# Performance work log

Hardware: AMD Instinct MI355X
Metric: run time of the kernel (lower is better)

The kernel has to match this reference:

```python
import jax, jax.numpy as jnp
import numpy as np

P = 2          # patch size
DEPTH = 3
NHEAD = 8
DROP_RATIO = 0.15
LN_EPS = 1e-5


def _ln(x, g, b):
    m = jnp.mean(x, axis=-1, keepdims=True)
    v = jnp.mean((x - m) ** 2, axis=-1, keepdims=True)
    return (x - m) * jax.lax.rsqrt(v + LN_EPS) * g + b


def setup_inputs() -> dict:
    key = jax.random.key(0)
    ks = jax.random.split(key, 16)
    B, C, HW, D, L = 4, 3, 96, 256, DEPTH
    N = (HW // P) ** 2
    s = 0.02
    return {
        "x": jax.random.normal(ks[0], (B, C, HW, HW), jnp.float32),
        "patch_w": jax.random.normal(ks[1], (D, C, P, P), jnp.float32) * s,
        "patch_b": jnp.zeros((D,), jnp.float32),
        "pos": jax.random.normal(ks[2], (1, N, D), jnp.float32) * s,
        "imp_w1": jax.random.normal(ks[3], (D, 256), jnp.float32) * s,
        "imp_b1": jnp.zeros((256,), jnp.float32),
        "imp_w2": jax.random.normal(ks[4], (256, 1), jnp.float32) * s,
        "imp_b2": jnp.zeros((1,), jnp.float32),
        "ln1_g": jnp.ones((L, D), jnp.float32),
        "ln1_b": jnp.zeros((L, D), jnp.float32),
        "qkv_w": jax.random.normal(ks[5], (L, D, 3 * D), jnp.float32) * s,
        "qkv_b": jnp.zeros((L, 3 * D), jnp.float32),
        "proj_w": jax.random.normal(ks[6], (L, D, D), jnp.float32) * s,
        "proj_b": jnp.zeros((L, D), jnp.float32),
        "ln2_g": jnp.ones((L, D), jnp.float32),
        "ln2_b": jnp.zeros((L, D), jnp.float32),
        "mlp_w1": jax.random.normal(ks[7], (L, D, 4 * D), jnp.float32) * s,
        "mlp_b1": jnp.zeros((L, 4 * D), jnp.float32),
        "mlp_w2": jax.random.normal(ks[8], (L, 4 * D, D), jnp.float32) * s,
        "mlp_b2": jnp.zeros((L, D), jnp.float32),
        "out_g": jnp.ones((D,), jnp.float32),
        "out_b": jnp.zeros((D,), jnp.float32),
    }


def reference(x, patch_w, patch_b, pos, imp_w1, imp_b1, imp_w2, imp_b2,
              ln1_g, ln1_b, qkv_w, qkv_b, proj_w, proj_b,
              ln2_g, ln2_b, mlp_w1, mlp_b1, mlp_w2, mlp_b2, out_g, out_b):
    B, C, H, W = x.shape
    D = patch_w.shape[0]
    Hc, Wc = H // P, W // P
    # Patch embed: conv(k=stride=P) == blocked einsum  -> (B, N, D)
    xr = x.reshape(B, C, Hc, P, Wc, P)
    tokens = jnp.einsum('bchpwq,dcpq->bhwd', xr, patch_w).reshape(B, Hc * Wc, D) + patch_b
    tokens = tokens + pos
    B, N, _ = tokens.shape

    # Importance scores -> bottom-k keys masked (Eq.8-10)
    h = jax.nn.relu(tokens @ imp_w1 + imp_b1)
    scores = jax.nn.sigmoid((h @ imp_w2 + imp_b2)[..., 0])  # (B, N)
    k = int(DROP_RATIO * N)
    _, idx = jax.lax.top_k(-scores, k)                      # k smallest scores
    md = jnp.zeros((B, N), bool).at[jnp.arange(B)[:, None], idx].set(True)

    dk = D // NHEAD
    scale = 1.0 / np.sqrt(dk)
    for l in range(DEPTH):
        hln = _ln(tokens, ln1_g[l], ln1_b[l])
        qkv = hln @ qkv_w[l] + qkv_b[l]
        q, kk, v = jnp.split(qkv, 3, axis=-1)
        q = q.reshape(B, N, NHEAD, dk).transpose(0, 2, 1, 3)
        kk = kk.reshape(B, N, NHEAD, dk).transpose(0, 2, 1, 3)
        v = v.reshape(B, N, NHEAD, dk).transpose(0, 2, 1, 3)
        logits = jnp.einsum('bhnd,bhmd->bhnm', q, kk) * scale
        logits = jnp.where(md[:, None, None, :], -jnp.inf, logits)
        attn = jax.nn.softmax(logits, axis=-1)
        out = jnp.einsum('bhnm,bhmd->bhnd', attn, v)
        out = out.transpose(0, 2, 1, 3).reshape(B, N, D)
        tokens = tokens + (out @ proj_w[l] + proj_b[l])
        h2 = _ln(tokens, ln2_g[l], ln2_b[l])
        tokens = tokens + (jax.nn.gelu(h2 @ mlp_w1[l] + mlp_b1[l], approximate=False) @ mlp_w2[l] + mlp_b2[l])

    tokens = _ln(tokens, out_g, out_b)
    return tokens.mean(axis=1)  # (B, D)
```

## Files before the change

### kernel.cpp

```cpp
#include <hip/hip_runtime.h>
#include <hip/hip_bf16.h>
#include <math.h>

#define BATCH 4
#define NTOK  2304
#define DIM   256
#define NHEADS 8
#define HCDIM 48
#define KSEL  345
#define NKEEP 1959
#define NKC   1984
#define KT    31
#define KREM  39
#define LN_EPS 1e-5f

typedef unsigned short u16;
typedef __attribute__((ext_vector_type(8))) short bf16x8;
typedef __attribute__((ext_vector_type(4))) float f32x4;

__device__ __forceinline__ u16 f2bf(float x) {
  union { float f; unsigned u; } v; v.f = x;
  return (u16)((v.u + 0x7FFFu + ((v.u >> 16) & 1u)) >> 16);
}

__device__ __forceinline__ void gload_lds16(const u16* g, u16* l) {
  __builtin_amdgcn_global_load_lds((const __attribute__((address_space(1))) void*)g,
                                   (__attribute__((address_space(3))) void*)l, 16, 0, 0);
}

__global__ __launch_bounds__(256) void k_patch_embed(
    const float* __restrict__ x, const float* __restrict__ pw,
    const float* __restrict__ pb, const float* __restrict__ pos,
    float* __restrict__ tokens) {
  int blk = blockIdx.x;
  int b = blk / NTOK, n = blk % NTOK;
  int hc = n / HCDIM, wc = n % HCDIM;
  __shared__ float xs[12];
  int t = threadIdx.x;
  if (t < 12) {
    int c = t >> 2, p = (t >> 1) & 1, q = t & 1;
    xs[t] = x[((b * 3 + c) * 96 + (hc * 2 + p)) * 96 + (wc * 2 + q)];
  }
  __syncthreads();
  float acc = pb[t];
#pragma unroll
  for (int i = 0; i < 12; ++i) acc += xs[i] * pw[t * 12 + i];
  tokens[(size_t)(b * NTOK + n) * DIM + t] = acc + pos[n * DIM + t];
}

__global__ __launch_bounds__(256) void k_importance(
    const float* __restrict__ tokens, const float* __restrict__ w1,
    const float* __restrict__ b1, const float* __restrict__ w2,
    const float* __restrict__ b2, float* __restrict__ scores) {
  __shared__ float ts[16 * 256];
  __shared__ float hw[16 * 256];
  int base = blockIdx.x * 16;
  int t = threadIdx.x;
  for (int i = t; i < 16 * 256; i += 256) ts[i] = tokens[(size_t)base * 256 + i];
  __syncthreads();
  float acc[16];
#pragma unroll
  for (int r = 0; r < 16; ++r) acc[r] = b1[t];
  for (int i = 0; i < 256; ++i) {
    float w = w1[i * 256 + t];
#pragma unroll
    for (int r = 0; r < 16; ++r) acc[r] += ts[r * 256 + i] * w;
  }
  float w2v = w2[t];
#pragma unroll
  for (int r = 0; r < 16; ++r) hw[r * 256 + t] = fmaxf(acc[r], 0.f) * w2v;
  __syncthreads();
  if (t < 16) {
    float s = b2[0];
    for (int i = 0; i < 256; ++i) s += hw[t * 256 + i];
    scores[base + t] = 1.f / (1.f + expf(-s));
  }
}

__global__ __launch_bounds__(256) void k_select(const float* __restrict__ scores,
                                                int* __restrict__ cmap,
                                                u16* __restrict__ kvc) {
  int b = blockIdx.x, t = threadIdx.x;
  __shared__ unsigned sb[NTOK];
  __shared__ int cnt;
  __shared__ int pfl[256], pfe[256];
  __shared__ int remS;
  for (int i = t; i < NTOK; i += 256) sb[i] = __float_as_uint(scores[b * NTOK + i]);
  __syncthreads();
  unsigned prefix = 0;
  int r = KSEL;
  for (int bit = 31; bit >= 0; --bit) {
    if (t == 0) cnt = 0;
    __syncthreads();
    unsigned bmask = 1u << bit;
    unsigned hmask = (bit == 31) ? 0u : ~((bmask << 1) - 1u);
    int local = 0;
    for (int i = t; i < NTOK; i += 256)
      if ((sb[i] & hmask) == prefix && !(sb[i] & bmask)) local++;
    if (local) atomicAdd(&cnt, local);
    __syncthreads();
    int c0 = cnt;
    if (r > c0) { r -= c0; prefix |= bmask; }
    __syncthreads();
  }
  unsigned v = prefix;
  int cl = 0, ce = 0;
  int j0 = t * 9;
  for (int j = j0; j < j0 + 9; ++j) { cl += (sb[j] < v); ce += (sb[j] == v); }
  pfl[t] = cl; pfe[t] = ce;
  __syncthreads();
  if (t == 0) {
    int pl = 0, pe = 0;
    for (int i = 0; i < 256; ++i) {
      int a = pfl[i], e = pfe[i];
      pfl[i] = pl; pfe[i] = pe;
      pl += a; pe += e;
    }
    remS = KSEL - pl;
  }
  __syncthreads();
  int pl = pfl[t], pe = pfe[t], rem = remS;
  for (int j = j0; j < j0 + 9; ++j) {
    bool less = sb[j] < v, eq = sb[j] == v;
    bool drop = less || (eq && pe < rem);
    int dropped_before = pl + (pe < rem ? pe : rem);
    cmap[b * NTOK + j] = drop ? -1 : (j - dropped_before);
    pl += less; pe += eq;
  }
  for (int i = t; i < (NKC - NKEEP) * 512; i += 256)
    kvc[((size_t)b * NKC + NKEEP) * 512 + i] = 0;
}

__global__ __launch_bounds__(256) void k_ln4bf(
    const float* __restrict__ in, u16* __restrict__ out,
    const float* __restrict__ g, const float* __restrict__ bta) {
  int w = threadIdx.x >> 6, l = threadIdx.x & 63;
  size_t row = (size_t)blockIdx.x * 4 + w;
  float4 v = *(const float4*)(in + row * DIM + l * 4);
  float s = v.x + v.y + v.z + v.w;
  float ss = v.x * v.x + v.y * v.y + v.z * v.z + v.w * v.w;
#pragma unroll
  for (int o = 1; o < 64; o <<= 1) { s += __shfl_xor(s, o); ss += __shfl_xor(ss, o); }
  float m = s * (1.f / DIM);
  float inv = rsqrtf(ss * (1.f / DIM) - m * m + LN_EPS);
  float4 gv = *(const float4*)(g + l * 4);
  float4 bv = *(const float4*)(bta + l * 4);
  union { ushort4 u4; __hip_bfloat162 h2[2]; } o4;
  o4.h2[0] = __float22bfloat162_rn(make_float2((v.x - m) * inv * gv.x + bv.x,
                                               (v.y - m) * inv * gv.y + bv.y));
  o4.h2[1] = __float22bfloat162_rn(make_float2((v.z - m) * inv * gv.z + bv.z,
                                               (v.w - m) * inv * gv.w + bv.w));
  *(ushort4*)(out + row * DIM + l * 4) = o4.u4;
}

__global__ __launch_bounds__(256) void k_lnmean(
    const float* __restrict__ in, const float* __restrict__ g,
    const float* __restrict__ bta, float* __restrict__ part) {
  int chunk = blockIdx.x, b = blockIdx.y;
  int w = threadIdx.x >> 6, l = threadIdx.x & 63;
  float4 gv = *(const float4*)(g + l * 4);
  float4 bv = *(const float4*)(bta + l * 4);
  float4 acc = make_float4(0.f, 0.f, 0.f, 0.f);
  for (int i = 0; i < 16; ++i) {
    size_t row = (size_t)b * NTOK + chunk * 64 + w * 16 + i;
    float4 v = *(const float4*)(in + row * DIM + l * 4);
    float s = v.x + v.y + v.z + v.w;
    float ss = v.x * v.x + v.y * v.y + v.z * v.z + v.w * v.w;
#pragma unroll
    for (int o = 1; o < 64; o <<= 1) { s += __shfl_xor(s, o); ss += __shfl_xor(ss, o); }
    float m = s * (1.f / DIM);
    float inv = rsqrtf(ss * (1.f / DIM) - m * m + LN_EPS);
    acc.x += (v.x - m) * inv * gv.x + bv.x;
    acc.y += (v.y - m) * inv * gv.y + bv.y;
    acc.z += (v.z - m) * inv * gv.z + bv.z;
    acc.w += (v.w - m) * inv * gv.w + bv.w;
  }
  __shared__ float4 red[4][64];
  red[w][l] = acc;
  __syncthreads();
  if (w == 0) {
    float4 a0 = red[0][l], a1 = red[1][l], a2 = red[2][l], a3 = red[3][l];
    float4 tot = make_float4(a0.x + a1.x + a2.x + a3.x, a0.y + a1.y + a2.y + a3.y,
                             a0.z + a1.z + a2.z + a3.z, a0.w + a1.w + a2.w + a3.w);
    *(float4*)(part + ((size_t)b * 36 + chunk) * DIM + l * 4) = tot;
  }
}

__global__ __launch_bounds__(256) void k_mean_final(const float* __restrict__ part,
                                                    float* __restrict__ out) {
  int b = blockIdx.x, d = threadIdx.x;
  float s = 0.f;
  for (int c = 0; c < 36; ++c) s += part[(size_t)(b * 36 + c) * DIM + d];
  out[b * DIM + d] = s * (1.0f / NTOK);
}

__global__ __launch_bounds__(256) void k_wtrans_all(
    const float* __restrict__ qkv_w, const float* __restrict__ proj_w,
    const float* __restrict__ mlp_w1, const float* __restrict__ mlp_w2,
    u16* __restrict__ wq, u16* __restrict__ wp,
    u16* __restrict__ w1, u16* __restrict__ w2) {
  int id = blockIdx.x;
  const float* W; u16* WT; int K, N, m;
  if (id < 576)       { m = id;        K = 256;  N = 768;  W = qkv_w;  WT = wq; }
  else if (id < 768)  { m = id - 576;  K = 256;  N = 256;  W = proj_w; WT = wp; }
  else if (id < 1536) { m = id - 768;  K = 256;  N = 1024; W = mlp_w1; WT = w1; }
  else                { m = id - 1536; K = 1024; N = 256;  W = mlp_w2; WT = w2; }
  int ntiles = N / 32, tilesPerLayer = ntiles * (K / 32);
  int layer = m / tilesPerLayer, tid = m % tilesPerLayer;
  int nb = (tid % ntiles) * 32, kb = (tid / ntiles) * 32;
  const float* Wl = W + (size_t)layer * K * N;
  u16* WTl = WT + (size_t)layer * K * N;
  __shared__ float tile[32][33];
  int tx = threadIdx.x & 31, ty = threadIdx.x >> 5;
  for (int i = 0; i < 32; i += 8) tile[ty + i][tx] = Wl[(size_t)(kb + ty + i) * N + nb + tx];
  __syncthreads();
  for (int i = 0; i < 32; i += 8)
    WTl[(size_t)(nb + ty + i) * K + kb + tx] = f2bf(tile[tx][ty + i]);
}

__global__ __launch_bounds__(256) void k_gemm_bf16(
    const u16* __restrict__ A, const u16* __restrict__ BT,
    const float* __restrict__ bias, u16* __restrict__ outb,
    int K, int N, int act) {
  __shared__ __align__(16) u16 As[2][128 * 32];
  __shared__ __align__(16) u16 Bs[2][128 * 32];
  int t = threadIdx.x;
  int m0 = blockIdx.y * 128, n0 = blockIdx.x * 128;
  int w = t >> 6, l = t & 63, lr = l & 15, qd = l >> 4;
  int wm = (w >> 1) * 64, wn = (w & 1) * 64;
  const u16* gA = A + (size_t)(m0 + w * 16 + (l >> 2)) * K + (l & 3) * 8;
  const u16* gA2 = gA + (size_t)64 * K;
  const u16* gB = BT + (size_t)(n0 + w * 16 + (l >> 2)) * K + (l & 3) * 8;
  const u16* gB2 = gB + (size_t)64 * K;
  f32x4 acc[4][4];
#pragma unroll
  for (int i = 0; i < 4; ++i)
#pragma unroll
    for (int j = 0; j < 4; ++j)
#pragma unroll
      for (int r = 0; r < 4; ++r) acc[i][j][r] = 0.f;
  gload_lds16(gA, As[0] + w * 512);
  gload_lds16(gA2, As[0] + 2048 + w * 512);
  gload_lds16(gB, Bs[0] + w * 512);
  gload_lds16(gB2, Bs[0] + 2048 + w * 512);
  int nchunks = K >> 5;
  for (int c = 0; c < nchunks; ++c) {
    int buf = c & 1;
    __syncthreads();
    if (c + 1 < nchunks) {
      int k0 = (c + 1) << 5;
      gload_lds16(gA + k0, As[buf ^ 1] + w * 512);
      gload_lds16(gA2 + k0, As[buf ^ 1] + 2048 + w * 512);
      gload_lds16(gB + k0, Bs[buf ^ 1] + w * 512);
      gload_lds16(gB2 + k0, Bs[buf ^ 1] + 2048 + w * 512);
    }
    bf16x8 af[4], bfr[4];
#pragma unroll
    for (int mt = 0; mt < 4; ++mt)
      af[mt] = *(const bf16x8*)(As[buf] + (wm + mt * 16 + lr) * 32 + qd * 8);
#pragma unroll
    for (int nt = 0; nt < 4; ++nt)
      bfr[nt] = *(const bf16x8*)(Bs[buf] + (wn + nt * 16 + lr) * 32 + qd * 8);
#pragma unroll
    for (int mt = 0; mt < 4; ++mt)
#pragma unroll
      for (int nt = 0; nt < 4; ++nt)
        acc[mt][nt] = __builtin_amdgcn_mfma_f32_16x16x32_bf16(af[mt], bfr[nt],
                                                              acc[mt][nt], 0, 0, 0);
  }
#pragma unroll
  for (int mt = 0; mt < 4; ++mt) {
#pragma unroll
    for (int nt = 0; nt < 4; ++nt) {
#pragma unroll
      for (int r = 0; r < 4; ++r) {
        size_t m = (size_t)m0 + wm + mt * 16 + qd * 4 + r;
        int c = n0 + wn + nt * 16 + lr;
        float val = acc[mt][nt][r] + bias[c];
        if (act) val = 0.5f * val * (1.f + erff(val * 0.70710678118654752f));
        outb[m * N + c] = f2bf(val);
      }
    }
  }
}

__global__ __launch_bounds__(256) void k_gemm_qkv(
    const u16* __restrict__ A, const u16* __restrict__ BT,
    const float* __restrict__ bias, const int* __restrict__ cmap,
    u16* __restrict__ Qb, u16* __restrict__ KVc) {
  const int K = 256, N = 768;
  __shared__ __align__(16) u16 As[2][128 * 32];
  __shared__ __align__(16) u16 Bs[2][128 * 32];
  int t = threadIdx.x;
  int m0 = blockIdx.y * 128, n0 = blockIdx.x * 128;
  int w = t >> 6, l = t & 63, lr = l & 15, qd = l >> 4;
  int wm = (w >> 1) * 64, wn = (w & 1) * 64;
  const u16* gA = A + (size_t)(m0 + w * 16 + (l >> 2)) * K + (l & 3) * 8;
  const u16* gA2 = gA + (size_t)64 * K;
  const u16* gB = BT + (size_t)(n0 + w * 16 + (l >> 2)) * K + (l & 3) * 8;
  const u16* gB2 = gB + (size_t)64 * K;
  f32x4 acc[4][4];
#pragma unroll
  for (int i = 0; i < 4; ++i)
#pragma unroll
    for (int j = 0; j < 4; ++j)
#pragma unroll
      for (int r = 0; r < 4; ++r) acc[i][j][r] = 0.f;
  gload_lds16(gA, As[0] + w * 512);
  gload_lds16(gA2, As[0] + 2048 + w * 512);
  gload_lds16(gB, Bs[0] + w * 512);
  gload_lds16(gB2, Bs[0] + 2048 + w * 512);
  for (int c = 0; c < 8; ++c) {
    int buf = c & 1;
    __syncthreads();
    if (c + 1 < 8) {
      int k0 = (c + 1) << 5;
      gload_lds16(gA + k0, As[buf ^ 1] + w * 512);
      gload_lds16(gA2 + k0, As[buf ^ 1] + 2048 + w * 512);
      gload_lds16(gB + k0, Bs[buf ^ 1] + w * 512);
      gload_lds16(gB2 + k0, Bs[buf ^ 1] + 2048 + w * 512);
    }
    bf16x8 af[4], bfr[4];
#pragma unroll
    for (int mt = 0; mt < 4; ++mt)
      af[mt] = *(const bf16x8*)(As[buf] + (wm + mt * 16 + lr) * 32 + qd * 8);
#pragma unroll
    for (int nt = 0; nt < 4; ++nt)
      bfr[nt] = *(const bf16x8*)(Bs[buf] + (wn + nt * 16 + lr) * 32 + qd * 8);
#pragma unroll
    for (int mt = 0; mt < 4; ++mt)
#pragma unroll
      for (int nt = 0; nt < 4; ++nt)
        acc[mt][nt] = __builtin_amdgcn_mfma_f32_16x16x32_bf16(af[mt], bfr[nt],
                                                              acc[mt][nt], 0, 0, 0);
  }
  bool isQ = (n0 + wn) < 256;
#pragma unroll
  for (int mt = 0; mt < 4; ++mt) {
#pragma unroll
    for (int r = 0; r < 4; ++r) {
      int m = m0 + wm + mt * 16 + qd * 4 + r;
      int cpos = isQ ? 0 : cmap[m];
      int b = m / NTOK;
#pragma unroll
      for (int nt = 0; nt < 4; ++nt) {
        int c = n0 + wn + nt * 16 + lr;
        float val = acc[mt][nt][r] + bias[c];
        if (isQ) {
          Qb[(size_t)m * 256 + c] = f2bf(val * 0.17677669529663687f);
        } else if (cpos >= 0) {
          KVc[((size_t)b * NKC + cpos) * 512 + (c - 256)] = f2bf(val);
        }
      }
    }
  }
}

__global__ __launch_bounds__(256) void k_gemm_n64(
    const u16* __restrict__ A, const u16* __restrict__ BT,
    const float* __restrict__ bias, const float* __restrict__ res,
    float* __restrict__ outf, int K, int N) {
  __shared__ __align__(16) u16 As[2][128 * 32];
  __shared__ __align__(16) u16 Bs[2][64 * 32];
  int t = threadIdx.x;
  int m0 = blockIdx.y * 128, n0 = blockIdx.x * 64;
  int w = t >> 6, l = t & 63, lr = l & 15, qd = l >> 4;
  int wm = (w >> 1) * 64, wn = (w & 1) * 32;
  const u16* gA = A + (size_t)(m0 + w * 16 + (l >> 2)) * K + (l & 3) * 8;
  const u16* gA2 = gA + (size_t)64 * K;
  const u16* gB = BT + (size_t)(n0 + w * 16 + (l >> 2)) * K + (l & 3) * 8;
  f32x4 acc[4][2];
#pragma unroll
  for (int i = 0; i < 4; ++i)
#pragma unroll
    for (int j = 0; j < 2; ++j)
#pragma unroll
      for (int r = 0; r < 4; ++r) acc[i][j][r] = 0.f;
  gload_lds16(gA, As[0] + w * 512);
  gload_lds16(gA2, As[0] + 2048 + w * 512);
  gload_lds16(gB, Bs[0] + w * 512);
  int nchunks = K >> 5;
  for (int c = 0; c < nchunks; ++c) {
    int buf = c & 1;
    __syncthreads();
    if (c + 1 < nchunks) {
      int k0 = (c + 1) << 5;
      gload_lds16(gA + k0, As[buf ^ 1] + w * 512);
      gload_lds16(gA2 + k0, As[buf ^ 1] + 2048 + w * 512);
      gload_lds16(gB + k0, Bs[buf ^ 1] + w * 512);
    }
    bf16x8 af[4], bfr[2];
#pragma unroll
    for (int mt = 0; mt < 4; ++mt)
      af[mt] = *(const bf16x8*)(As[buf] + (wm + mt * 16 + lr) * 32 + qd * 8);
#pragma unroll
    for (int nt = 0; nt < 2; ++nt)
      bfr[nt] = *(const bf16x8*)(Bs[buf] + (wn + nt * 16 + lr) * 32 + qd * 8);
#pragma unroll
    for (int mt = 0; mt < 4; ++mt)
#pragma unroll
      for (int nt = 0; nt < 2; ++nt)
        acc[mt][nt] = __builtin_amdgcn_mfma_f32_16x16x32_bf16(af[mt], bfr[nt],
                                                              acc[mt][nt], 0, 0, 0);
  }
#pragma unroll
  for (int mt = 0; mt < 4; ++mt) {
#pragma unroll
    for (int nt = 0; nt < 2; ++nt) {
#pragma unroll
      for (int r = 0; r < 4; ++r) {
        size_t m = (size_t)m0 + wm + mt * 16 + qd * 4 + r;
        int c = n0 + wn + nt * 16 + lr;
        outf[m * N + c] = acc[mt][nt][r] + bias[c] + res[m * N + c];
      }
    }
  }
}

__global__ __launch_bounds__(256) void k_attn4(
    const u16* __restrict__ Qb, const u16* __restrict__ KVc,
    u16* __restrict__ outb) {
  int qt = blockIdx.x, h = blockIdx.y, b = blockIdx.z;
  int t = threadIdx.x, w = t >> 6, l = t & 63, lr = l & 15, qd = l >> 4;
  __shared__ __align__(16) u16 Ks[2][64 * 32];
  __shared__ __align__(16) u16 Vt[2][32][80];
  __shared__ __align__(16) u16 Pq[4][32][80];
  const short ONE = (short)0x3F80;
  int q0 = qt * 128 + w * 32;
  const u16* kvb = KVc + (size_t)b * NKC * 512;
  bf16x8 qf[2];
  qf[0] = *(const bf16x8*)(Qb + ((size_t)(b * NTOK) + q0 + lr) * 256 + h * 32 + qd * 8);
  qf[1] = *(const bf16x8*)(Qb + ((size_t)(b * NTOK) + q0 + 16 + lr) * 256 + h * 32 + qd * 8);
  const u16* gK = kvb + (size_t)(t >> 2) * 512 + h * 32 + (t & 3) * 8;
  const u16* gV = kvb + (size_t)l * 512 + 256 + h * 32 + w * 8;
  gload_lds16(gK, &Ks[0][w * 512]);
  bf16x8 vr = *(const bf16x8*)(gV);
  f32x4 oa[2][2];
  f32x4 lacc[2];
#pragma unroll
  for (int r = 0; r < 4; ++r) {
    oa[0][0][r] = 0.f; oa[0][1][r] = 0.f; oa[1][0][r] = 0.f; oa[1][1][r] = 0.f;
    lacc[0][r] = 0.f; lacc[1][r] = 0.f;
  }
  bf16x8 ones;
#pragma unroll
  for (int j = 0; j < 8; ++j) ones[j] = ONE;
  for (int kt = 0; kt < KT; ++kt) {
    int buf = kt & 1;
#pragma unroll
    for (int j = 0; j < 8; ++j) Vt[buf][w * 8 + j][l] = (u16)vr[j];
    __syncthreads();
    if (kt + 1 < KT) {
      size_t off = (size_t)(kt + 1) * 64 * 512;
      gload_lds16(gK + off, &Ks[buf ^ 1][w * 512]);
      vr = *(const bf16x8*)(gV + off);
    }
    bf16x8 kf[4];
#pragma unroll
    for (int nt = 0; nt < 4; ++nt)
      kf[nt] = *(const bf16x8*)(&Ks[buf][(nt * 16 + lr) * 32 + qd * 8]);
#pragma unroll
    for (int qh = 0; qh < 2; ++qh) {
      f32x4 p4[4];
#pragma unroll
      for (int nt = 0; nt < 4; ++nt) {
        f32x4 z; z[0] = 0.f; z[1] = 0.f; z[2] = 0.f; z[3] = 0.f;
        p4[nt] = __builtin_amdgcn_mfma_f32_16x16x32_bf16(kf[nt], qf[qh], z, 0, 0, 0);
      }
#pragma unroll
      for (int nt = 0; nt < 4; ++nt)
#pragma unroll
        for (int r = 0; r < 4; ++r) p4[nt][r] = __expf(p4[nt][r]);
#pragma unroll
      for (int nt = 0; nt < 4; ++nt) {
        union { ushort4 u4; __hip_bfloat162 h2[2]; } pu;
        pu.h2[0] = __float22bfloat162_rn(make_float2(p4[nt][0], p4[nt][1]));
        pu.h2[1] = __float22bfloat162_rn(make_float2(p4[nt][2], p4[nt][3]));
        *(ushort4*)(&Pq[w][qh * 16 + lr][nt * 16 + qd * 4]) = pu.u4;
      }
    }
    bf16x8 of1 = ones;
    if (kt == KT - 1) {
#pragma unroll
      for (int j = 0; j < 8; ++j) of1[j] = (32 + qd * 8 + j < KREM) ? ONE : (short)0;
    }
#pragma unroll
    for (int qh = 0; qh < 2; ++qh) {
#pragma unroll
      for (int kh = 0; kh < 2; ++kh) {
        bf16x8 pf = *(const bf16x8*)(&Pq[w][qh * 16 + lr][kh * 32 + qd * 8]);
#pragma unroll
        for (int dh = 0; dh < 2; ++dh) {
          bf16x8 vf = *(const bf16x8*)(&Vt[buf][dh * 16 + lr][kh * 32 + qd * 8]);
          oa[qh][dh] = __builtin_amdgcn_mfma_f32_16x16x32_bf16(pf, vf, oa[qh][dh], 0, 0, 0);
        }
        lacc[qh] = __builtin_amdgcn_mfma_f32_16x16x32_bf16(
            pf, kh ? of1 : ones, lacc[qh], 0, 0, 0);
      }
    }
  }
#pragma unroll
  for (int qh = 0; qh < 2; ++qh) {
#pragma unroll
    for (int r = 0; r < 4; ++r) {
      float inv = 1.f / lacc[qh][r];
      size_t row = (size_t)b * NTOK + q0 + qh * 16 + qd * 4 + r;
      outb[row * 256 + h * 32 + lr] = f2bf(oa[qh][0][r] * inv);
      outb[row * 256 + h * 32 + 16 + lr] = f2bf(oa[qh][1][r] * inv);
    }
  }
}

extern "C" void kernel_launch(void* const* d_in, const int* in_sizes, int n_in,
                              void* d_out, int out_size, void* d_ws, size_t ws_size,
                              hipStream_t stream) {
  (void)in_sizes; (void)n_in; (void)out_size;
  const float* x       = (const float*)d_in[0];
  const float* patch_w = (const float*)d_in[1];
  const float* patch_b = (const float*)d_in[2];
  const float* pos     = (const float*)d_in[3];
  const float* imp_w1  = (const float*)d_in[4];
  const float* imp_b1  = (const float*)d_in[5];
  const float* imp_w2  = (const float*)d_in[6];
  const float* imp_b2  = (const float*)d_in[7];
  const float* ln1_g   = (const float*)d_in[8];
  const float* ln1_b   = (const float*)d_in[9];
  const float* qkv_w   = (const float*)d_in[10];
  const float* qkv_b   = (const float*)d_in[11];
  const float* proj_w  = (const float*)d_in[12];
  const float* proj_b  = (const float*)d_in[13];
  const float* ln2_g   = (const float*)d_in[14];
  const float* ln2_b   = (const float*)d_in[15];
  const float* mlp_w1  = (const float*)d_in[16];
  const float* mlp_b1  = (const float*)d_in[17];
  const float* mlp_w2  = (const float*)d_in[18];
  const float* mlp_b2  = (const float*)d_in[19];
  const float* out_g   = (const float*)d_in[20];
  const float* out_b   = (const float*)d_in[21];
  float* out = (float*)d_out;

  const int M = BATCH * NTOK;
  const size_t TOK = (size_t)M * DIM;

  char* p = (char*)d_ws;
  float* tokens = (float*)p;       p += TOK * 4;
  float* scoresp = (float*)p;      p += (size_t)M * 4;
  int* cmap = (int*)p;             p += (size_t)M * 4;
  u16* act_bf = (u16*)p;           p += TOK * 2;
  u16* Qb = (u16*)p;               p += TOK * 2;
  u16* kvc = (u16*)p;              p += (size_t)BATCH * NKC * 512 * 2;
  u16* big_bf = (u16*)p;           p += (size_t)M * 1024 * 2;
  u16* wq_t = (u16*)p;             p += (size_t)3 * 768 * 256 * 2;
  u16* wp_t = (u16*)p;             p += (size_t)3 * 256 * 256 * 2;
  u16* w1_t = (u16*)p;             p += (size_t)3 * 1024 * 256 * 2;
  u16* w2_t = (u16*)p;             p += (size_t)3 * 256 * 1024 * 2;
  float* partials = (float*)act_bf;
  if (ws_size < (size_t)(p - (char*)d_ws)) return;

  k_wtrans_all<<<dim3(2304), 256, 0, stream>>>(qkv_w, proj_w, mlp_w1, mlp_w2,
                                               wq_t, wp_t, w1_t, w2_t);
  k_patch_embed<<<dim3(M), 256, 0, stream>>>(x, patch_w, patch_b, pos, tokens);
  k_importance<<<dim3(M / 16), 256, 0, stream>>>(tokens, imp_w1, imp_b1, imp_w2, imp_b2, scoresp);
  k_select<<<dim3(BATCH), 256, 0, stream>>>(scoresp, cmap, kvc);

  for (int l = 0; l < 3; ++l) {
    k_ln4bf<<<dim3(M / 4), 256, 0, stream>>>(tokens, act_bf, ln1_g + l * DIM, ln1_b + l * DIM);
    k_gemm_qkv<<<dim3(6, 72), 256, 0, stream>>>(
        act_bf, wq_t + (size_t)l * 768 * 256, qkv_b + l * 768, cmap, Qb, kvc);
    k_attn4<<<dim3(18, NHEADS, BATCH), 256, 0, stream>>>(Qb, kvc, act_bf);
    k_gemm_n64<<<dim3(4, 72), 256, 0, stream>>>(
        act_bf, wp_t + (size_t)l * 256 * 256, proj_b + l * DIM, tokens, tokens, 256, 256);
    k_ln4bf<<<dim3(M / 4), 256, 0, stream>>>(tokens, act_bf, ln2_g + l * DIM, ln2_b + l * DIM);
    k_gemm_bf16<<<dim3(8, 72), 256, 0, stream>>>(
        act_bf, w1_t + (size_t)l * 1024 * 256, mlp_b1 + l * 1024, big_bf, 256, 1024, 1);
    k_gemm_n64<<<dim3(4, 72), 256, 0, stream>>>(
        big_bf, w2_t + (size_t)l * 256 * 1024, mlp_b2 + l * DIM, tokens, tokens, 1024, 256);
  }
  k_lnmean<<<dim3(36, BATCH), 256, 0, stream>>>(tokens, out_g, out_b, partials);
  k_mean_final<<<dim3(BATCH), 256, 0, stream>>>(partials, out);
}
```

Baseline: 613.6 us.

## Split K/V buffers, store V transposed, load attention fragments from global, halve n64 tile

Result: slower. 690.8 us (+12.6%).

```diff
diff --git a/kernel.cpp b/kernel.cpp
--- a/kernel.cpp
+++ b/kernel.cpp
@@ -79,7 +79,8 @@
 
 __global__ __launch_bounds__(256) void k_select(const float* __restrict__ scores,
                                                 int* __restrict__ cmap,
-                                                u16* __restrict__ kvc) {
+                                                u16* __restrict__ Kc,
+                                                u16* __restrict__ VT) {
   int b = blockIdx.x, t = threadIdx.x;
   __shared__ unsigned sb[NTOK];
   __shared__ int cnt;
@@ -127,8 +128,12 @@
     cmap[b * NTOK + j] = drop ? -1 : (j - dropped_before);
     pl += less; pe += eq;
   }
-  for (int i = t; i < (NKC - NKEEP) * 512; i += 256)
-    kvc[((size_t)b * NKC + NKEEP) * 512 + i] = 0;
+  for (int i = t; i < (NKC - NKEEP) * 256; i += 256)
+    Kc[((size_t)b * NKC + NKEEP) * 256 + i] = 0;
+  for (int i = t; i < 256 * (NKC - NKEEP); i += 256) {
+    int row = i / (NKC - NKEEP), key = i % (NKC - NKEEP);
+    VT[((size_t)b * 256 + row) * NKC + NKEEP + key] = 0;
+  }
 }
 
 __global__ __launch_bounds__(256) void k_ln4bf(
@@ -287,7 +292,7 @@
 __global__ __launch_bounds__(256) void k_gemm_qkv(
     const u16* __restrict__ A, const u16* __restrict__ BT,
     const float* __restrict__ bias, const int* __restrict__ cmap,
-    u16* __restrict__ Qb, u16* __restrict__ KVc) {
+    u16* __restrict__ Qb, u16* __restrict__ Kc, u16* __restrict__ VT) {
   const int K = 256, N = 768;
   __shared__ __align__(16) u16 As[2][128 * 32];
   __shared__ __align__(16) u16 Bs[2][128 * 32];
@@ -334,22 +339,26 @@
         acc[mt][nt] = __builtin_amdgcn_mfma_f32_16x16x32_bf16(af[mt], bfr[nt],
                                                               acc[mt][nt], 0, 0, 0);
   }
-  bool isQ = (n0 + wn) < 256;
+  int sec = (n0 + wn) >> 8;
 #pragma unroll
   for (int mt = 0; mt < 4; ++mt) {
 #pragma unroll
     for (int r = 0; r < 4; ++r) {
       int m = m0 + wm + mt * 16 + qd * 4 + r;
-      int cpos = isQ ? 0 : cmap[m];
+      int cpos = (sec == 0) ? 0 : cmap[m];
       int b = m / NTOK;
 #pragma unroll
       for (int nt = 0; nt < 4; ++nt) {
         int c = n0 + wn + nt * 16 + lr;
         float val = acc[mt][nt][r] + bias[c];
-        if (isQ) {
-          Qb[(size_t)m * 256 + c] = f2bf(val * 0.17677669529663687f);
+        if (sec == 0) {
+          Qb[(size_t)m * 256 + c] = f2bf(val * 0.25508688726880056f);
         } else if (cpos >= 0) {
-          KVc[((size_t)b * NKC + cpos) * 512 + (c - 256)] = f2bf(val);
+          if (sec == 1) {
+            Kc[((size_t)b * NKC + cpos) * 256 + (c - 256)] = f2bf(val);
+          } else {
+            VT[((size_t)b * 256 + (c - 512)) * NKC + cpos] = f2bf(val);
+          }
         }
       }
     }
@@ -360,24 +369,22 @@
     const u16* __restrict__ A, const u16* __restrict__ BT,
     const float* __restrict__ bias, const float* __restrict__ res,
     float* __restrict__ outf, int K, int N) {
-  __shared__ __align__(16) u16 As[2][128 * 32];
+  __shared__ __align__(16) u16 As[2][64 * 32];
   __shared__ __align__(16) u16 Bs[2][64 * 32];
   int t = threadIdx.x;
-  int m0 = blockIdx.y * 128, n0 = blockIdx.x * 64;
+  int m0 = blockIdx.y * 64, n0 = blockIdx.x * 64;
   int w = t >> 6, l = t & 63, lr = l & 15, qd = l >> 4;
-  int wm = (w >> 1) * 64, wn = (w & 1) * 32;
+  int wm = (w >> 1) * 32, wn = (w & 1) * 32;
   const u16* gA = A + (size_t)(m0 + w * 16 + (l >> 2)) * K + (l & 3) * 8;
-  const u16* gA2 = gA + (size_t)64 * K;
   const u16* gB = BT + (size_t)(n0 + w * 16 + (l >> 2)) * K + (l & 3) * 8;
-  f32x4 acc[4][2];
-#pragma unroll
-  for (int i = 0; i < 4; ++i)
+  f32x4 acc[2][2];
+#pragma unroll
+  for (int i = 0; i < 2; ++i)
 #pragma unroll
     for (int j = 0; j < 2; ++j)
 #pragma unroll
       for (int r = 0; r < 4; ++r) acc[i][j][r] = 0.f;
   gload_lds16(gA, As[0] + w * 512);
-  gload_lds16(gA2, As[0] + 2048 + w * 512);
   gload_lds16(gB, Bs[0] + w * 512);
   int nchunks = K >> 5;
   for (int c = 0; c < nchunks; ++c) {
@@ -386,25 +393,24 @@
     if (c + 1 < nchunks) {
       int k0 = (c + 1) << 5;
       gload_lds16(gA + k0, As[buf ^ 1] + w * 512);
-      gload_lds16(gA2 + k0, As[buf ^ 1] + 2048 + w * 512);
       gload_lds16(gB + k0, Bs[buf ^ 1] + w * 512);
     }
-    bf16x8 af[4], bfr[2];
-#pragma unroll
-    for (int mt = 0; mt < 4; ++mt)
+    bf16x8 af[2], bfr[2];
+#pragma unroll
+    for (int mt = 0; mt < 2; ++mt)
       af[mt] = *(const bf16x8*)(As[buf] + (wm + mt * 16 + lr) * 32 + qd * 8);
 #pragma unroll
     for (int nt = 0; nt < 2; ++nt)
       bfr[nt] = *(const bf16x8*)(Bs[buf] + (wn + nt * 16 + lr) * 32 + qd * 8);
 #pragma unroll
-    for (int mt = 0; mt < 4; ++mt)
+    for (int mt = 0; mt < 2; ++mt)
 #pragma unroll
       for (int nt = 0; nt < 2; ++nt)
         acc[mt][nt] = __builtin_amdgcn_mfma_f32_16x16x32_bf16(af[mt], bfr[nt],
                                                               acc[mt][nt], 0, 0, 0);
   }
 #pragma unroll
-  for (int mt = 0; mt < 4; ++mt) {
+  for (int mt = 0; mt < 2; ++mt) {
 #pragma unroll
     for (int nt = 0; nt < 2; ++nt) {
 #pragma unroll
@@ -417,24 +423,19 @@
   }
 }
 
-__global__ __launch_bounds__(256) void k_attn4(
-    const u16* __restrict__ Qb, const u16* __restrict__ KVc,
-    u16* __restrict__ outb) {
+__global__ __launch_bounds__(256) void k_attn5(
+    const u16* __restrict__ Qb, const u16* __restrict__ Kc,
+    const u16* __restrict__ VT, u16* __restrict__ outb) {
   int qt = blockIdx.x, h = blockIdx.y, b = blockIdx.z;
   int t = threadIdx.x, w = t >> 6, l = t & 63, lr = l & 15, qd = l >> 4;
-  __shared__ __align__(16) u16 Ks[2][64 * 32];
-  __shared__ __align__(16) u16 Vt[2][32][80];
-  __shared__ __align__(16) u16 Pq[4][32][80];
+  __shared__ __align__(16) u16 Pq[4][16][80];
   const short ONE = (short)0x3F80;
   int q0 = qt * 128 + w * 32;
-  const u16* kvb = KVc + (size_t)b * NKC * 512;
+  const u16* kcb = Kc + (size_t)b * NKC * 256 + h * 32;
+  const u16* vtb = VT + ((size_t)b * 256 + h * 32) * NKC;
   bf16x8 qf[2];
   qf[0] = *(const bf16x8*)(Qb + ((size_t)(b * NTOK) + q0 + lr) * 256 + h * 32 + qd * 8);
   qf[1] = *(const bf16x8*)(Qb + ((size_t)(b * NTOK) + q0 + 16 + lr) * 256 + h * 32 + qd * 8);
-  const u16* gK = kvb + (size_t)(t >> 2) * 512 + h * 32 + (t & 3) * 8;
-  const u16* gV = kvb + (size_t)l * 512 + 256 + h * 32 + w * 8;
-  gload_lds16(gK, &Ks[0][w * 512]);
-  bf16x8 vr = *(const bf16x8*)(gV);
   f32x4 oa[2][2];
   f32x4 lacc[2];
 #pragma unroll
@@ -445,58 +446,68 @@
   bf16x8 ones;
 #pragma unroll
   for (int j = 0; j < 8; ++j) ones[j] = ONE;
+  bf16x8 kfc[4], vfc[4], kfn[4], vfn[4];
+#pragma unroll
+  for (int nt = 0; nt < 4; ++nt)
+    kfc[nt] = *(const bf16x8*)(kcb + (size_t)(nt * 16 + lr) * 256 + qd * 8);
+#pragma unroll
+  for (int kh = 0; kh < 2; ++kh)
+#pragma unroll
+    for (int dh = 0; dh < 2; ++dh)
+      vfc[kh * 2 + dh] = *(const bf16x8*)(vtb + (size_t)(dh * 16 + lr) * NKC + kh * 32 + qd * 8);
   for (int kt = 0; kt < KT; ++kt) {
-    int buf = kt & 1;
-#pragma unroll
-    for (int j = 0; j < 8; ++j) Vt[buf][w * 8 + j][l] = (u16)vr[j];
-    __syncthreads();
     if (kt + 1 < KT) {
-      size_t off = (size_t)(kt + 1) * 64 * 512;
-      gload_lds16(gK + off, &Ks[buf ^ 1][w * 512]);
-      vr = *(const bf16x8*)(gV + off);
-    }
-    bf16x8 kf[4];
-#pragma unroll
-    for (int nt = 0; nt < 4; ++nt)
-      kf[nt] = *(const bf16x8*)(&Ks[buf][(nt * 16 + lr) * 32 + qd * 8]);
+      int kb = (kt + 1) * 64;
+#pragma unroll
+      for (int nt = 0; nt < 4; ++nt)
+        kfn[nt] = *(const bf16x8*)(kcb + (size_t)(kb + nt * 16 + lr) * 256 + qd * 8);
+#pragma unroll
+      for (int kh = 0; kh < 2; ++kh)
+#pragma unroll
+        for (int dh = 0; dh < 2; ++dh)
+          vfn[kh * 2 + dh] =
+              *(const bf16x8*)(vtb + (size_t)(dh * 16 + lr) * NKC + kb + kh * 32 + qd * 8);
+    }
+    bf16x8 of1 = ones;
+    if (kt == KT - 1) {
+#pragma unroll
+      for (int j = 0; j < 8; ++j) of1[j] = (32 + qd * 8 + j < KREM) ? ONE : (short)0;
+    }
 #pragma unroll
     for (int qh = 0; qh < 2; ++qh) {
       f32x4 p4[4];
 #pragma unroll
       for (int nt = 0; nt < 4; ++nt) {
         f32x4 z; z[0] = 0.f; z[1] = 0.f; z[2] = 0.f; z[3] = 0.f;
-        p4[nt] = __builtin_amdgcn_mfma_f32_16x16x32_bf16(kf[nt], qf[qh], z, 0, 0, 0);
+        p4[nt] = __builtin_amdgcn_mfma_f32_16x16x32_bf16(kfc[nt], qf[qh], z, 0, 0, 0);
       }
 #pragma unroll
       for (int nt = 0; nt < 4; ++nt)
 #pragma unroll
-        for (int r = 0; r < 4; ++r) p4[nt][r] = __expf(p4[nt][r]);
+        for (int r = 0; r < 4; ++r) p4[nt][r] = __builtin_amdgcn_exp2f(p4[nt][r]);
 #pragma unroll
       for (int nt = 0; nt < 4; ++nt) {
         union { ushort4 u4; __hip_bfloat162 h2[2]; } pu;
         pu.h2[0] = __float22bfloat162_rn(make_float2(p4[nt][0], p4[nt][1]));
         pu.h2[1] = __float22bfloat162_rn(make_float2(p4[nt][2], p4[nt][3]));
-        *(ushort4*)(&Pq[w][qh * 16 + lr][nt * 16 + qd * 4]) = pu.u4;
+        *(ushort4*)(&Pq[w][lr][nt * 16 + qd * 4]) = pu.u4;
       }
-    }
-    bf16x8 of1 = ones;
-    if (kt == KT - 1) {
-#pragma unroll
-      for (int j = 0; j < 8; ++j) of1[j] = (32 + qd * 8 + j < KREM) ? ONE : (short)0;
-    }
-#pragma unroll
-    for (int qh = 0; qh < 2; ++qh) {
 #pragma unroll
       for (int kh = 0; kh < 2; ++kh) {
-        bf16x8 pf = *(const bf16x8*)(&Pq[w][qh * 16 + lr][kh * 32 + qd * 8]);
-#pragma unroll
-        for (int dh = 0; dh < 2; ++dh) {
-          bf16x8 vf = *(const bf16x8*)(&Vt[buf][dh * 16 + lr][kh * 32 + qd * 8]);
-          oa[qh][dh] = __builtin_amdgcn_mfma_f32_16x16x32_bf16(pf, vf, oa[qh][dh], 0, 0, 0);
-        }
-        lacc[qh] = __builtin_amdgcn_mfma_f32_16x16x32_bf16(
-            pf, kh ? of1 : ones, lacc[qh], 0, 0, 0);
+        bf16x8 pf = *(const bf16x8*)(&Pq[w][lr][kh * 32 + qd * 8]);
+#pragma unroll
+        for (int dh = 0; dh < 2; ++dh)
+          oa[qh][dh] = __builtin_amdgcn_mfma_f32_16x16x32_bf16(pf, vfc[kh * 2 + dh],
+                                                               oa[qh][dh], 0, 0, 0);
+        lacc[qh] = __builtin_amdgcn_mfma_f32_16x16x32_bf16(pf, kh ? of1 : ones,
+                                                           lacc[qh], 0, 0, 0);
       }
+    }
+    if (kt + 1 < KT) {
+#pragma unroll
+      for (int nt = 0; nt < 4; ++nt) kfc[nt] = kfn[nt];
+#pragma unroll
+      for (int i = 0; i < 4; ++i) vfc[i] = vfn[i];
     }
   }
 #pragma unroll
@@ -548,7 +559,8 @@
   int* cmap = (int*)p;             p += (size_t)M * 4;
   u16* act_bf = (u16*)p;           p += TOK * 2;
   u16* Qb = (u16*)p;               p += TOK * 2;
-  u16* kvc = (u16*)p;              p += (size_t)BATCH * NKC * 512 * 2;
+  u16* kc = (u16*)p;               p += (size_t)BATCH * NKC * 256 * 2;
+  u16* vt = (u16*)p;               p += (size_t)BATCH * 256 * NKC * 2;
   u16* big_bf = (u16*)p;           p += (size_t)M * 1024 * 2;
   u16* wq_t = (u16*)p;             p += (size_t)3 * 768 * 256 * 2;
   u16* wp_t = (u16*)p;             p += (size_t)3 * 256 * 256 * 2;
@@ -561,19 +573,19 @@
                                                wq_t, wp_t, w1_t, w2_t);
   k_patch_embed<<<dim3(M), 256, 0, stream>>>(x, patch_w, patch_b, pos, tokens);
   k_importance<<<dim3(M / 16), 256, 0, stream>>>(tokens, imp_w1, imp_b1, imp_w2, imp_b2, scoresp);
-  k_select<<<dim3(BATCH), 256, 0, stream>>>(scoresp, cmap, kvc);
+  k_select<<<dim3(BATCH), 256, 0, stream>>>(scoresp, cmap, kc, vt);
 
   for (int l = 0; l < 3; ++l) {
     k_ln4bf<<<dim3(M / 4), 256, 0, stream>>>(tokens, act_bf, ln1_g + l * DIM, ln1_b + l * DIM);
     k_gemm_qkv<<<dim3(6, 72), 256, 0, stream>>>(
-        act_bf, wq_t + (size_t)l * 768 * 256, qkv_b + l * 768, cmap, Qb, kvc);
-    k_attn4<<<dim3(18, NHEADS, BATCH), 256, 0, stream>>>(Qb, kvc, act_bf);
-    k_gemm_n64<<<dim3(4, 72), 256, 0, stream>>>(
+        act_bf, wq_t + (size_t)l * 768 * 256, qkv_b + l * 768, cmap, Qb, kc, vt);
+    k_attn5<<<dim3(18, NHEADS, BATCH), 256, 0, stream>>>(Qb, kc, vt, act_bf);
+    k_gemm_n64<<<dim3(4, 144), 256, 0, stream>>>(
         act_bf, wp_t + (size_t)l * 256 * 256, proj_b + l * DIM, tokens, tokens, 256, 256);
     k_ln4bf<<<dim3(M / 4), 256, 0, stream>>>(tokens, act_bf, ln2_g + l * DIM, ln2_b + l * DIM);
     k_gemm_bf16<<<dim3(8, 72), 256, 0, stream>>>(
         act_bf, w1_t + (size_t)l * 1024 * 256, mlp_b1 + l * 1024, big_bf, 256, 1024, 1);
-    k_gemm_n64<<<dim3(4, 72), 256, 0, stream>>>(
+    k_gemm_n64<<<dim3(4, 144), 256, 0, stream>>>(
         big_bf, w2_t + (size_t)l * 256 * 1024, mlp_b2 + l * DIM, tokens, tokens, 1024, 256);
   }
   k_lnmean<<<dim3(36, BATCH), 256, 0, stream>>>(tokens, out_g, out_b, partials);
```
